# Performance work log

Measured on AMD Instinct MI355X. Metric: run time of the kernel, lower is better.

Reference implementation:

```python
import jax, jax.numpy as jnp
from jax import lax
import numpy as np

N = 32768; K = 8; M = 8192; G = 32; EF = 128

def _lrelu(x):
    return jnp.where(x > 0, x, 0.01 * x)

def _pc_res(x, W1, b1, W2, b2):
    h = _lrelu(x @ W1 + b1) @ W2 + b2
    return _lrelu(h + x)

def _conv3d(x, w, b):
    dn = ('NCDHW', 'OIDHW', 'NCDHW')
    return lax.conv_general_dilated(x, w, (1, 1, 1), 'SAME', dimension_numbers=dn) + b[None, :, None, None, None]

def setup_inputs():
    key = jax.random.key(0)
    ks = jax.random.split(key, 32)
    f32 = jnp.float32
    pc_KNN_idx = jax.random.randint(ks[0], (N * K,), 0, N, dtype=jnp.int32)
    pc_KNN_xyz = jax.random.normal(ks[1], (N * K, 3), dtype=f32)
    flat = jax.random.permutation(ks[2], G * G * G)[:M]  # unique voxel coords -> deterministic scatter
    voxel_xyz_int = jnp.stack([flat // (G * G), (flat // G) % G, flat % G], axis=1).astype(jnp.int32)
    voxel_KNN_idx = jax.random.randint(ks[3], (M * K,), 0, N, dtype=jnp.int32)
    voxel_KNN_xyz = jax.random.normal(ks[4], (M * K, 3), dtype=f32)
    s = 0.05
    def rn(i, shape):
        return jax.random.normal(ks[i], shape, dtype=f32) * s
    return dict(
        pc_KNN_idx=pc_KNN_idx, pc_KNN_xyz=pc_KNN_xyz, voxel_xyz_int=voxel_xyz_int,
        voxel_KNN_idx=voxel_KNN_idx, voxel_KNN_xyz=voxel_KNN_xyz,
        pcf_W1=rn(5, (3, EF)), pcf_b1=rn(6, (EF,)), pcf_W2=rn(7, (EF, EF)), pcf_b2=rn(8, (EF,)),
        pcres_W1=rn(9, (7, EF, EF)), pcres_b1=rn(10, (7, EF)),
        pcres_W2=rn(11, (7, EF, EF)), pcres_b2=rn(12, (7, EF)),
        pcc_W1=rn(13, (6, EF + 3, EF)), pcc_b1=rn(14, (6, EF)),
        pcc_W2=rn(15, (6, EF, EF)), pcc_b2=rn(16, (6, EF)),
        r3_Wc1=rn(17, (8, EF, EF, 3, 3, 3)), r3_bc1=rn(18, (8, EF)),
        r3_Wc2=rn(19, (8, EF, EF, 1, 1, 1)), r3_bc2=rn(20, (8, EF)),
        lin1_W=rn(21, (EF, EF)), lin1_b=rn(22, (EF,)),
        lin2_W=rn(23, (EF, EF)), lin2_b=rn(24, (EF,)),
        linb_W=rn(25, (EF, 3)), linb_b=rn(26, (3,)),
    )

def reference(pc_KNN_idx, pc_KNN_xyz, voxel_xyz_int, voxel_KNN_idx, voxel_KNN_xyz,
              pcf_W1, pcf_b1, pcf_W2, pcf_b2,
              pcres_W1, pcres_b1, pcres_W2, pcres_b2,
              pcc_W1, pcc_b1, pcc_W2, pcc_b2,
              r3_Wc1, r3_bc1, r3_Wc2, r3_bc2,
              lin1_W, lin1_b, lin2_W, lin2_b, linb_W, linb_b):
    # pc_conv_first: MLP on KNN relative xyz, max-pool over K neighbors -> [N, EF]
    out = _lrelu(pc_KNN_xyz @ pcf_W1 + pcf_b1) @ pcf_W2 + pcf_b2
    out = jnp.max(out.reshape(-1, K, EF), axis=1)
    out = _lrelu(out)
    out = _pc_res(out, pcres_W1[0], pcres_b1[0], pcres_W2[0], pcres_b2[0])
    for i in range(6):
        idx = pc_KNN_idx if i < 5 else voxel_KNN_idx
        xyz = pc_KNN_xyz if i < 5 else voxel_KNN_xyz
        g = jnp.concatenate([out[idx], xyz], axis=1)            # [R*K, EF+3]
        h = _lrelu(g @ pcc_W1[i] + pcc_b1[i]) @ pcc_W2[i] + pcc_b2[i]
        out = _lrelu(jnp.max(h.reshape(-1, K, EF), axis=1))     # [R, EF]
        out = _pc_res(out, pcres_W1[i + 1], pcres_b1[i + 1], pcres_W2[i + 1], pcres_b2[i + 1])
    # scatter voxel features into a dense grid (coords are unique)
    vi = voxel_xyz_int - jnp.min(voxel_xyz_int, axis=0)
    grid = jnp.zeros((G, G, G, EF), jnp.float32).at[vi[:, 0], vi[:, 1], vi[:, 2]].set(out)
    x = grid.transpose(3, 0, 1, 2)[None]                        # [1, EF, G, G, G]
    for i in range(8):
        y = _lrelu(_conv3d(x, r3_Wc1[i], r3_bc1[i]))
        y = _conv3d(y, r3_Wc2[i], r3_bc2[i])
        x = _lrelu(y + x)
    out = x[0].transpose(1, 2, 3, 0)[vi[:, 0], vi[:, 1], vi[:, 2]]  # gather back [M, EF]
    out = _lrelu(out @ lin1_W + lin1_b)
    out = _lrelu(out @ lin2_W + lin2_b)
    return jax.nn.sigmoid(out @ linb_W + linb_b)                # out_bool head [M, 3]
```

## Files before the change

kernel.cpp:

```cpp
#include <hip/hip_runtime.h>
#include <math.h>

#define EF 128
#define NPTS 32768
#define KNN 8
#define MVOX 8192
#define GDIM 32
#define NVOXG (GDIM*GDIM*GDIM)

typedef __attribute__((ext_vector_type(8))) short bfrag;
typedef __attribute__((ext_vector_type(4))) float f32x4;

__device__ __forceinline__ float lrelu(float x) { return x > 0.f ? x : 0.01f * x; }
__device__ __forceinline__ short f2b(float f) {
    unsigned u = __float_as_uint(f);
    return (short)((u + 0x7fff + ((u >> 16) & 1)) >> 16);
}
#define MFMA(a,b,c) __builtin_amdgcn_mfma_f32_16x16x32_bf16((a),(b),(c),0,0,0)
__device__ __forceinline__ int swz(int row, int bytecol) {
    return row * 256 + (bytecol ^ ((row & 7) << 4));
}

__global__ void k_pack_w(const float* __restrict__ src, short* __restrict__ dst,
                         int K_real, int n_steps, int k_str, int c_str,
                         int src_ls, int dst_ls, int n_layers) {
    int t = blockIdx.x * 256 + threadIdx.x;
    int per = n_steps * 4096;
    if (t >= n_layers * per) return;
    int layer = t / per;
    int u = t - layer * per;
    int r = u & 7, l = (u >> 3) & 63, ct = (u >> 9) & 7, s = u >> 12;
    int k = s * 32 + (l >> 4) * 8 + r;
    int col = ct * 16 + (l & 15);
    float v = (k < K_real) ? src[(size_t)layer * src_ls + (size_t)k * k_str + (size_t)col * c_str] : 0.f;
    dst[(size_t)layer * dst_ls + u] = f2b(v);
}
__global__ void k_pack_wc1(const float* __restrict__ src, short* __restrict__ dst) {
    int g = blockIdx.x;
    int layer = g / 1728;
    int t = (g - layer * 1728) * 256 + threadIdx.x;
    if (t >= 108 * 4096) return;
    int r = t & 7, l = (t >> 3) & 63, ct = (t >> 9) & 7, s = t >> 12;
    int tap = s >> 2;
    int ci = (s & 3) * 32 + (l >> 4) * 8 + r;
    int col = ct * 16 + (l & 15);
    dst[(size_t)layer * 442368 + t] =
        f2b(src[(size_t)layer * 442368 + ((size_t)col * 128 + ci) * 27 + tap]);
}


__global__ __launch_bounds__(512) void k_pcfirst(
    const float* __restrict__ xyz, const short* __restrict__ w1p, const float* __restrict__ b1,
    const short* __restrict__ w2p, const float* __restrict__ b2,
    const short* __restrict__ rw1p, const float* __restrict__ rb1,
    const short* __restrict__ rw2p, const float* __restrict__ rb2,
    float* __restrict__ out32, short* __restrict__ out16) {
    __shared__ __align__(16) char tb[32768];
    int wid = threadIdx.x >> 6, lane = threadIdx.x & 63, lrow = lane & 15, lq = lane >> 4;
    int wm = wid >> 2, wn = wid & 3;
    int rowbase = blockIdx.x * 128;
    f32x4 zv = {0.f, 0.f, 0.f, 0.f};
    {
        f32x4 acc1[4][2];
        #pragma unroll
        for (int rt = 0; rt < 4; ++rt) { acc1[rt][0] = zv; acc1[rt][1] = zv; }
        bfrag Bv[2];
        #pragma unroll
        for (int ct = 0; ct < 2; ++ct) Bv[ct] = ((const bfrag*)w1p)[(wn * 2 + ct) * 64 + lane];
        #pragma unroll
        for (int rt = 0; rt < 4; ++rt) {
            bfrag a4;
            #pragma unroll
            for (int r = 0; r < 8; ++r) a4[r] = 0;
            if (lq == 0) {
                int gr = rowbase + wm * 64 + rt * 16 + lrow;
                a4[0] = f2b(xyz[gr * 3]); a4[1] = f2b(xyz[gr * 3 + 1]); a4[2] = f2b(xyz[gr * 3 + 2]);
            }
            #pragma unroll
            for (int ct = 0; ct < 2; ++ct) acc1[rt][ct] = MFMA(a4, Bv[ct], acc1[rt][ct]);
        }
        float bb1[2];
        #pragma unroll
        for (int ct = 0; ct < 2; ++ct) bb1[ct] = b1[wn * 32 + ct * 16 + lrow];
        #pragma unroll
        for (int rt = 0; rt < 4; ++rt)
            #pragma unroll
            for (int ct = 0; ct < 2; ++ct)
                #pragma unroll
                for (int r = 0; r < 4; ++r) {
                    int row = wm * 64 + rt * 16 + lq * 4 + r, col = wn * 32 + ct * 16 + lrow;
                    *(short*)(tb + swz(row, col * 2)) = f2b(lrelu(acc1[rt][ct][r] + bb1[ct]));
                }
    }
    __syncthreads();
    float bb2[2];
    #pragma unroll
    for (int ct = 0; ct < 2; ++ct) bb2[ct] = b2[wn * 32 + ct * 16 + lrow];
    f32x4 acc[4][2];
    #pragma unroll
    for (int rt = 0; rt < 4; ++rt) { acc[rt][0] = zv; acc[rt][1] = zv; }
    const bfrag* bp2 = (const bfrag*)w2p;
    #pragma unroll
    for (int s = 0; s < 4; ++s) {
        bfrag Bv[2];
        #pragma unroll
        for (int ct = 0; ct < 2; ++ct) Bv[ct] = bp2[(s * 8 + wn * 2 + ct) * 64 + lane];
        bfrag av[4];
        #pragma unroll
        for (int rt = 0; rt < 4; ++rt) {
            int row = wm * 64 + rt * 16 + lrow;
            av[rt] = *(const bfrag*)(tb + swz(row, s * 64 + lq * 16));
        }
        #pragma unroll
        for (int ct = 0; ct < 2; ++ct)
            #pragma unroll
            for (int rt = 0; rt < 4; ++rt) acc[rt][ct] = MFMA(av[rt], Bv[ct], acc[rt][ct]);
    }
    float pv[4][2];
    #pragma unroll
    for (int rt = 0; rt < 4; ++rt)
        #pragma unroll
        for (int ct = 0; ct < 2; ++ct) {
            float m = -INFINITY;
            #pragma unroll
            for (int r = 0; r < 4; ++r) m = fmaxf(m, acc[rt][ct][r] + bb2[ct]);
            m = fmaxf(m, __shfl_xor(m, 16, 64));
            pv[rt][ct] = lrelu(m);
        }
    __syncthreads();
    float* xf = (float*)(tb + 4096);
    char*  tres = tb + 12544;
    if ((lq & 1) == 0) {
        #pragma unroll
        for (int rt = 0; rt < 4; ++rt)
            #pragma unroll
            for (int ct = 0; ct < 2; ++ct) {
                int row = wm * 8 + rt * 2 + (lq >> 1), col = wn * 32 + ct * 16 + lrow;
                *(short*)(tb + swz(row, col * 2)) = f2b(pv[rt][ct]);
                xf[row * 130 + col] = pv[rt][ct];
            }
    }
    __syncthreads();
    {
        f32x4 r1 = zv;
        #pragma unroll
        for (int s = 0; s < 4; ++s) {
            bfrag B = ((const bfrag*)rw1p)[(s * 8 + wid) * 64 + lane];
            bfrag a = *(const bfrag*)(tb + swz(lrow, s * 64 + lq * 16));
            r1 = MFMA(a, B, r1);
        }
        float rb1v = rb1[wid * 16 + lrow];
        #pragma unroll
        for (int r = 0; r < 4; ++r) {
            int row = lq * 4 + r;
            *(short*)(tres + swz(row, (wid * 16 + lrow) * 2)) = f2b(lrelu(r1[r] + rb1v));
        }
    }
    __syncthreads();
    {
        f32x4 r2 = zv;
        #pragma unroll
        for (int s = 0; s < 4; ++s) {
            bfrag B = ((const bfrag*)rw2p)[(s * 8 + wid) * 64 + lane];
            bfrag a = *(const bfrag*)(tres + swz(lrow, s * 64 + lq * 16));
            r2 = MFMA(a, B, r2);
        }
        float rb2v = rb2[wid * 16 + lrow];
        int p0 = blockIdx.x * 16;
        #pragma unroll
        for (int r = 0; r < 4; ++r) {
            int row = lq * 4 + r, col = wid * 16 + lrow;
            float v = lrelu(r2[r] + rb2v + xf[row * 130 + col]);
            size_t o = (size_t)(p0 + row) * 128 + col;
            out16[o] = f2b(v);
            if (out32) out32[o] = v;
        }
    }
}

__global__ __launch_bounds__(512) void k_pcconv(
    const short* __restrict__ fin16, const int* __restrict__ idx, const float* __restrict__ xyz,
    const short* __restrict__ w1p, const float* __restrict__ b1,
    const short* __restrict__ w2p, const float* __restrict__ b2,
    const short* __restrict__ rw1p, const float* __restrict__ rb1,
    const short* __restrict__ rw2p, const float* __restrict__ rb2,
    float* __restrict__ out32, short* __restrict__ out16) {
    __shared__ __align__(16) char tb[32768];
    int wid = threadIdx.x >> 6, lane = threadIdx.x & 63, lrow = lane & 15, lq = lane >> 4;
    int wm = wid >> 2, wn = wid & 3;
    int rowbase = blockIdx.x * 128;
    f32x4 zv = {0.f, 0.f, 0.f, 0.f};
    {
        int srow = threadIdx.x >> 2, sseg = threadIdx.x & 3;
        int nb = idx[rowbase + srow];
        const bfrag* src = (const bfrag*)(fin16 + (size_t)nb * 128);
        #pragma unroll
        for (int j = 0; j < 4; ++j) {
            int seg = sseg + j * 4;
            bfrag v = src[seg];
            *(bfrag*)(tb + swz(srow, seg * 16)) = v;
        }
    }
    __syncthreads();
    float bb1[2], bb2[2];
    #pragma unroll
    for (int ct = 0; ct < 2; ++ct) {
        bb1[ct] = b1[wn * 32 + ct * 16 + lrow];
        bb2[ct] = b2[wn * 32 + ct * 16 + lrow];
    }
    f32x4 acc[4][2];
    #pragma unroll
    for (int rt = 0; rt < 4; ++rt) { acc[rt][0] = zv; acc[rt][1] = zv; }
    const bfrag* bp1 = (const bfrag*)w1p;
    #pragma unroll
    for (int s = 0; s < 4; ++s) {
        bfrag Bv[2];
        #pragma unroll
        for (int ct = 0; ct < 2; ++ct) Bv[ct] = bp1[(s * 8 + wn * 2 + ct) * 64 + lane];
        bfrag av[4];
        #pragma unroll
        for (int rt = 0; rt < 4; ++rt) {
            int row = wm * 64 + rt * 16 + lrow;
            av[rt] = *(const bfrag*)(tb + swz(row, s * 64 + lq * 16));
        }
        #pragma unroll
        for (int ct = 0; ct < 2; ++ct)
            #pragma unroll
            for (int rt = 0; rt < 4; ++rt) acc[rt][ct] = MFMA(av[rt], Bv[ct], acc[rt][ct]);
    }
    {
        bfrag Bv[2];
        #pragma unroll
        for (int ct = 0; ct < 2; ++ct) Bv[ct] = bp1[(32 + wn * 2 + ct) * 64 + lane];
        #pragma unroll
        for (int rt = 0; rt < 4; ++rt) {
            bfrag a4;
            #pragma unroll
            for (int r = 0; r < 8; ++r) a4[r] = 0;
            if (lq == 0) {
                int gr = rowbase + wm * 64 + rt * 16 + lrow;
                a4[0] = f2b(xyz[gr * 3]); a4[1] = f2b(xyz[gr * 3 + 1]); a4[2] = f2b(xyz[gr * 3 + 2]);
            }
            #pragma unroll
            for (int ct = 0; ct < 2; ++ct) acc[rt][ct] = MFMA(a4, Bv[ct], acc[rt][ct]);
        }
    }
    __syncthreads();
    #pragma unroll
    for (int rt = 0; rt < 4; ++rt)
        #pragma unroll
        for (int ct = 0; ct < 2; ++ct)
            #pragma unroll
            for (int r = 0; r < 4; ++r) {
                int row = wm * 64 + rt * 16 + lq * 4 + r, col = wn * 32 + ct * 16 + lrow;
                *(short*)(tb + swz(row, col * 2)) = f2b(lrelu(acc[rt][ct][r] + bb1[ct]));
            }
    __syncthreads();
    f32x4 acc2[4][2];
    #pragma unroll
    for (int rt = 0; rt < 4; ++rt) { acc2[rt][0] = zv; acc2[rt][1] = zv; }
    const bfrag* bp2 = (const bfrag*)w2p;
    #pragma unroll
    for (int s = 0; s < 4; ++s) {
        bfrag Bv[2];
        #pragma unroll
        for (int ct = 0; ct < 2; ++ct) Bv[ct] = bp2[(s * 8 + wn * 2 + ct) * 64 + lane];
        bfrag av[4];
        #pragma unroll
        for (int rt = 0; rt < 4; ++rt) {
            int row = wm * 64 + rt * 16 + lrow;
            av[rt] = *(const bfrag*)(tb + swz(row, s * 64 + lq * 16));
        }
        #pragma unroll
        for (int ct = 0; ct < 2; ++ct)
            #pragma unroll
            for (int rt = 0; rt < 4; ++rt) acc2[rt][ct] = MFMA(av[rt], Bv[ct], acc2[rt][ct]);
    }
    float pv[4][2];
    #pragma unroll
    for (int rt = 0; rt < 4; ++rt)
        #pragma unroll
        for (int ct = 0; ct < 2; ++ct) {
            float m = -INFINITY;
            #pragma unroll
            for (int r = 0; r < 4; ++r) m = fmaxf(m, acc2[rt][ct][r] + bb2[ct]);
            m = fmaxf(m, __shfl_xor(m, 16, 64));
            pv[rt][ct] = lrelu(m);
        }
    __syncthreads();
    float* xf = (float*)(tb + 4096);
    char*  tres = tb + 12544;
    if ((lq & 1) == 0) {
        #pragma unroll
        for (int rt = 0; rt < 4; ++rt)
            #pragma unroll
            for (int ct = 0; ct < 2; ++ct) {
                int row = wm * 8 + rt * 2 + (lq >> 1), col = wn * 32 + ct * 16 + lrow;
                *(short*)(tb + swz(row, col * 2)) = f2b(pv[rt][ct]);
                xf[row * 130 + col] = pv[rt][ct];
            }
    }
    __syncthreads();
    {
        f32x4 r1 = zv;
        #pragma unroll
        for (int s = 0; s < 4; ++s) {
            bfrag B = ((const bfrag*)rw1p)[(s * 8 + wid) * 64 + lane];
            bfrag a = *(const bfrag*)(tb + swz(lrow, s * 64 + lq * 16));
            r1 = MFMA(a, B, r1);
        }
        float rb1v = rb1[wid * 16 + lrow];
        #pragma unroll
        for (int r = 0; r < 4; ++r) {
            int row = lq * 4 + r;
            *(short*)(tres + swz(row, (wid * 16 + lrow) * 2)) = f2b(lrelu(r1[r] + rb1v));
        }
    }
    __syncthreads();
    {
        f32x4 r2 = zv;
        #pragma unroll
        for (int s = 0; s < 4; ++s) {
            bfrag B = ((const bfrag*)rw2p)[(s * 8 + wid) * 64 + lane];
            bfrag a = *(const bfrag*)(tres + swz(lrow, s * 64 + lq * 16));
            r2 = MFMA(a, B, r2);
        }
        float rb2v = rb2[wid * 16 + lrow];
        int p0 = blockIdx.x * 16;
        #pragma unroll
        for (int r = 0; r < 4; ++r) {
            int row = lq * 4 + r, col = wid * 16 + lrow;
            float v = lrelu(r2[r] + rb2v + xf[row * 130 + col]);
            size_t o = (size_t)(p0 + row) * 128 + col;
            out16[o] = f2b(v);
            if (out32) out32[o] = v;
        }
    }
}

__global__ __launch_bounds__(512) void k_conv3(
    const float* __restrict__ gin32, const short* __restrict__ gin16,
    const short* __restrict__ w1p, const float* __restrict__ b1,
    const short* __restrict__ w2p, const float* __restrict__ b2,
    float* __restrict__ gout32, short* __restrict__ gout16) {
    __shared__ __align__(16) char Ab[65536];
    int wid = threadIdx.x >> 6, lane = threadIdx.x & 63, lrow = lane & 15, lq = lane >> 4;
    int kg = wid & 1, wn = (wid >> 1) & 1, wm = wid >> 2;
    int va = blockIdx.x >> 3, vb0 = (blockIdx.x & 7) * 4;
    bfrag zf;
    #pragma unroll
    for (int r = 0; r < 8; ++r) zf[r] = 0;
    f32x4 zv = {0.f, 0.f, 0.f, 0.f};
    f32x4 acc[4][4];
    #pragma unroll
    for (int rt = 0; rt < 4; ++rt)
        #pragma unroll
        for (int ct = 0; ct < 4; ++ct) acc[rt][ct] = zv;
    const bfrag* bp1 = (const bfrag*)w1p;

    #pragma unroll 1
    for (int dai = 0; dai < 3; ++dai) {
        __syncthreads();
        {
            int aa = va + dai - 1;
            bool aok = (unsigned)aa < 32u;
            #pragma unroll
            for (int j = 0; j < 6; ++j) {
                int task = (int)threadIdx.x + j * 512;
                int srow = task >> 4, seg = task & 15;
                int bl = srow >> 5, c = srow & 31;
                int sb = vb0 - 1 + bl;
                bool ok = aok && ((unsigned)sb < 32u);
                size_t gb = ok ? ((size_t)((aa * 32 + sb) * 32 + c) * 128 + seg * 8) : 0;
                bfrag v = *((const bfrag*)gin16 + gb / 8);
                *(bfrag*)(Ab + swz(srow, seg * 16)) = ok ? v : zf;
            }
        }
        __syncthreads();
        #pragma unroll
        for (int t9 = 0; t9 < 9; ++t9) {
            int db = t9 / 3 - 1, dc = t9 % 3 - 1;
            int tap = dai * 9 + t9;
            #pragma unroll
            for (int ss = 0; ss < 2; ++ss) {
                int s = kg * 2 + ss;
                bfrag Bv[4];
                #pragma unroll
                for (int ct = 0; ct < 4; ++ct)
                    Bv[ct] = bp1[((tap * 4 + s) * 8 + wn * 4 + ct) * 64 + lane];
                bfrag av[4];
                #pragma unroll
                for (int rt = 0; rt < 4; ++rt) {
                    int ci = ((rt & 1) << 4) + lrow + dc;
                    bool ok = (unsigned)ci < 32u;
                    int srow2 = (wm * 2 + db + 1 + (rt >> 1)) * 32 + (ok ? ci : 0);
                    bfrag t = *(const bfrag*)(Ab + swz(srow2, s * 64 + lq * 16));
                    av[rt] = ok ? t : zf;
                }
                #pragma unroll
                for (int ct = 0; ct < 4; ++ct)
                    #pragma unroll
                    for (int rt = 0; rt < 4; ++rt) acc[rt][ct] = MFMA(av[rt], Bv[ct], acc[rt][ct]);
            }
        }
    }
    __syncthreads();
    if (kg == 1) {
        int p = wm * 2 + wn;
        #pragma unroll
        for (int rt = 0; rt < 4; ++rt)
            #pragma unroll
            for (int ct = 0; ct < 4; ++ct)
                *(f32x4*)(Ab + p * 16384 + ((rt * 4 + ct) * 64 + lane) * 16) = acc[rt][ct];
    }
    __syncthreads();
    if (kg == 0) {
        int p = wm * 2 + wn;
        #pragma unroll
        for (int rt = 0; rt < 4; ++rt)
            #pragma unroll
            for (int ct = 0; ct < 4; ++ct)
                acc[rt][ct] += *(const f32x4*)(Ab + p * 16384 + ((rt * 4 + ct) * 64 + lane) * 16);
    }
    __syncthreads();
    if (kg == 0) {
        float bb1[4];
        #pragma unroll
        for (int ct = 0; ct < 4; ++ct) bb1[ct] = b1[wn * 64 + ct * 16 + lrow];
        #pragma unroll
        for (int rt = 0; rt < 4; ++rt)
            #pragma unroll
            for (int ct = 0; ct < 4; ++ct)
                #pragma unroll
                for (int r = 0; r < 4; ++r) {
                    int row = wm * 64 + rt * 16 + lq * 4 + r, col = wn * 64 + ct * 16 + lrow;
                    *(short*)(Ab + swz(row, col * 2)) = f2b(lrelu(acc[rt][ct][r] + bb1[ct]));
                }
    }
    __syncthreads();
    int wm2 = wid >> 2, wn2 = wid & 3;
    float bb2[2];
    #pragma unroll
    for (int ct = 0; ct < 2; ++ct) bb2[ct] = b2[wn2 * 32 + ct * 16 + lrow];
    f32x4 acc2[4][2];
    #pragma unroll
    for (int rt = 0; rt < 4; ++rt) { acc2[rt][0] = zv; acc2[rt][1] = zv; }
    const bfrag* bp2 = (const bfrag*)w2p;
    #pragma unroll
    for (int s = 0; s < 4; ++s) {
        bfrag Bv[2];
        #pragma unroll
        for (int ct = 0; ct < 2; ++ct) Bv[ct] = bp2[(s * 8 + wn2 * 2 + ct) * 64 + lane];
        bfrag av[4];
        #pragma unroll
        for (int rt = 0; rt < 4; ++rt) {
            int row = wm2 * 64 + rt * 16 + lrow;
            av[rt] = *(const bfrag*)(Ab + swz(row, s * 64 + lq * 16));
        }
        #pragma unroll
        for (int ct = 0; ct < 2; ++ct)
            #pragma unroll
            for (int rt = 0; rt < 4; ++rt) acc2[rt][ct] = MFMA(av[rt], Bv[ct], acc2[rt][ct]);
    }
    #pragma unroll
    for (int rt = 0; rt < 4; ++rt)
        #pragma unroll
        for (int ct = 0; ct < 2; ++ct)
            #pragma unroll
            for (int r = 0; r < 4; ++r) {
                int row = wm2 * 64 + rt * 16 + lq * 4 + r;
                int voxel = (va * 32 + vb0 + (row >> 5)) * 32 + (row & 31);
                size_t o = (size_t)voxel * 128 + wn2 * 32 + ct * 16 + lrow;
                float v = lrelu(acc2[rt][ct][r] + bb2[ct] + gin32[o]);
                gout32[o] = v; gout16[o] = f2b(v);
            }
}

__global__ __launch_bounds__(512) void k_head(
    const short* __restrict__ g16, const int* __restrict__ vx, const int* __restrict__ vmin,
    const short* __restrict__ w1p, const float* __restrict__ b1,
    const short* __restrict__ w2p, const float* __restrict__ b2,
    const float* __restrict__ W3, const float* __restrict__ b3,
    float* __restrict__ out) {
    __shared__ __align__(16) char tb[16384];
    __shared__ float t2[64][129];
    int wid = threadIdx.x >> 6, lane = threadIdx.x & 63, lrow = lane & 15, lq = lane >> 4;
    int rowbase = blockIdx.x * 64;
    int goff[4];
    #pragma unroll
    for (int rt = 0; rt < 4; ++rt) {
        int m = rowbase + rt * 16 + lrow;
        int v0 = vx[m * 3 + 0] - vmin[0];
        int v1 = vx[m * 3 + 1] - vmin[1];
        int v2 = vx[m * 3 + 2] - vmin[2];
        goff[rt] = ((v0 * 32 + v1) * 32 + v2) * 128;
    }
    float bb1 = b1[wid * 16 + lrow], bb2 = b2[wid * 16 + lrow];
    f32x4 zv = {0.f, 0.f, 0.f, 0.f};
    f32x4 acc[4];
    #pragma unroll
    for (int rt = 0; rt < 4; ++rt) acc[rt] = zv;
    const bfrag* bp1 = (const bfrag*)w1p;
    #pragma unroll
    for (int s = 0; s < 4; ++s) {
        bfrag B = bp1[(s * 8 + wid) * 64 + lane];
        #pragma unroll
        for (int rt = 0; rt < 4; ++rt) {
            bfrag a = *((const bfrag*)(g16 + goff[rt]) + s * 4 + lq);
            acc[rt] = MFMA(a, B, acc[rt]);
        }
    }
    #pragma unroll
    for (int rt = 0; rt < 4; ++rt)
        #pragma unroll
        for (int r = 0; r < 4; ++r) {
            int row = rt * 16 + lq * 4 + r, col = wid * 16 + lrow;
            *(short*)(tb + swz(row, col * 2)) = f2b(lrelu(acc[rt][r] + bb1));
        }
    __syncthreads();
    f32x4 acc2[4];
    #pragma unroll
    for (int rt = 0; rt < 4; ++rt) acc2[rt] = zv;
    const bfrag* bp2 = (const bfrag*)w2p;
    #pragma unroll
    for (int s = 0; s < 4; ++s) {
        bfrag B = bp2[(s * 8 + wid) * 64 + lane];
        #pragma unroll
        for (int rt = 0; rt < 4; ++rt) {
            int row = rt * 16 + lrow;
            bfrag av = *(const bfrag*)(tb + swz(row, s * 64 + lq * 16));
            acc2[rt] = MFMA(av, B, acc2[rt]);
        }
    }
    #pragma unroll
    for (int rt = 0; rt < 4; ++rt)
        #pragma unroll
        for (int r = 0; r < 4; ++r) {
            int row = rt * 16 + lq * 4 + r, col = wid * 16 + lrow;
            t2[row][col] = lrelu(acc2[rt][r] + bb2);
        }
    __syncthreads();
    if (threadIdx.x < 192) {
        int row = threadIdx.x & 63, c = threadIdx.x >> 6;
        float s = b3[c];
        #pragma unroll 4
        for (int k = 0; k < 128; ++k) s += t2[row][k] * W3[k * 3 + c];
        out[(size_t)(rowbase + row) * 3 + c] = 1.f / (1.f + expf(-s));
    }
}

__global__ void k_vmin(const int* __restrict__ vx, int M, int* __restrict__ vmin) {
    __shared__ int sm[3 * 256];
    int t = threadIdx.x;
    int m0 = 0x7fffffff, m1 = 0x7fffffff, m2 = 0x7fffffff;
    for (int i = t; i < M; i += 256) {
        m0 = min(m0, vx[i * 3 + 0]); m1 = min(m1, vx[i * 3 + 1]); m2 = min(m2, vx[i * 3 + 2]);
    }
    sm[t] = m0; sm[256 + t] = m1; sm[512 + t] = m2;
    __syncthreads();
    for (int s = 128; s > 0; s >>= 1) {
        if (t < s) {
            sm[t] = min(sm[t], sm[t + s]);
            sm[256 + t] = min(sm[256 + t], sm[256 + t + s]);
            sm[512 + t] = min(sm[512 + t], sm[512 + t + s]);
        }
        __syncthreads();
    }
    if (t == 0) { vmin[0] = sm[0]; vmin[1] = sm[256]; vmin[2] = sm[512]; }
}

__global__ void k_scatter(const float* __restrict__ vf, const int* __restrict__ vx,
                          const int* __restrict__ vmin, float* __restrict__ g32, short* __restrict__ g16) {
    int m = blockIdx.x, j = threadIdx.x;
    int v0 = vx[m * 3 + 0] - vmin[0];
    int v1 = vx[m * 3 + 1] - vmin[1];
    int v2 = vx[m * 3 + 2] - vmin[2];
    size_t o = (size_t)(((v0 * GDIM) + v1) * GDIM + v2) * EF + j;
    float v = vf[(size_t)m * EF + j];
    g32[o] = v; g16[o] = f2b(v);
}

extern "C" void kernel_launch(void* const* d_in, const int* in_sizes, int n_in,
                              void* d_out, int out_size, void* d_ws, size_t ws_size,
                              hipStream_t stream) {
    const int*   pc_idx  = (const int*)  d_in[0];
    const float* pc_xyz  = (const float*)d_in[1];
    const int*   vox_int = (const int*)  d_in[2];
    const int*   vox_idx = (const int*)  d_in[3];
    const float* vox_xyz = (const float*)d_in[4];
    const float* pcf_W1  = (const float*)d_in[5];
    const float* pcf_b1  = (const float*)d_in[6];
    const float* pcf_W2  = (const float*)d_in[7];
    const float* pcf_b2  = (const float*)d_in[8];
    const float* pcres_W1 = (const float*)d_in[9];
    const float* pcres_b1 = (const float*)d_in[10];
    const float* pcres_W2 = (const float*)d_in[11];
    const float* pcres_b2 = (const float*)d_in[12];
    const float* pcc_W1  = (const float*)d_in[13];
    const float* pcc_b1  = (const float*)d_in[14];
    const float* pcc_W2  = (const float*)d_in[15];
    const float* pcc_b2  = (const float*)d_in[16];
    const float* r3_Wc1  = (const float*)d_in[17];
    const float* r3_bc1  = (const float*)d_in[18];
    const float* r3_Wc2  = (const float*)d_in[19];
    const float* r3_bc2  = (const float*)d_in[20];
    const float* lin1_W  = (const float*)d_in[21];
    const float* lin1_b  = (const float*)d_in[22];
    const float* lin2_W  = (const float*)d_in[23];
    const float* lin2_b  = (const float*)d_in[24];
    const float* linb_W  = (const float*)d_in[25];
    const float* linb_b  = (const float*)d_in[26];

    const size_t NE = (size_t)NPTS * EF;
    float* A32 = (float*)d_ws;
    float* B32 = A32 + NE;
    short* A16 = (short*)(B32 + NE);
    short* B16 = A16 + NE;
    float* Y32 = (float*)(B16 + NE);
    short* Y16 = (short*)(Y32 + NE);
    short* pcf_w1p = Y16 + NE;
    short* pcf_w2p = pcf_w1p + 1 * 4096;
    short* pcc_w1p = pcf_w2p + 4 * 4096;
    short* pcc_w2p = pcc_w1p + 6 * 5 * 4096;
    short* pcr_w1p = pcc_w2p + 6 * 4 * 4096;
    short* pcr_w2p = pcr_w1p + 7 * 4 * 4096;
    short* wc2p    = pcr_w2p + 7 * 4 * 4096;
    short* lin1p   = wc2p    + 8 * 4 * 4096;
    short* lin2p   = lin1p   + 4 * 4096;
    short* wc1p    = lin2p   + 4 * 4096;
    int*   vmin    = (int*)(wc1p + 8 * 108 * 4096);

    k_pack_w<<<16, 256, 0, stream>>>(pcf_W1, pcf_w1p, 3, 1, 128, 1, 0, 0, 1);
    k_pack_w<<<64, 256, 0, stream>>>(pcf_W2, pcf_w2p, 128, 4, 128, 1, 0, 0, 1);
    k_pack_w<<<480, 256, 0, stream>>>(pcc_W1, pcc_w1p, 131, 5, 128, 1, 131 * 128, 5 * 4096, 6);
    k_pack_w<<<384, 256, 0, stream>>>(pcc_W2, pcc_w2p, 128, 4, 128, 1, 128 * 128, 4 * 4096, 6);
    k_pack_w<<<448, 256, 0, stream>>>(pcres_W1, pcr_w1p, 128, 4, 128, 1, 128 * 128, 4 * 4096, 7);
    k_pack_w<<<448, 256, 0, stream>>>(pcres_W2, pcr_w2p, 128, 4, 128, 1, 128 * 128, 4 * 4096, 7);
    k_pack_w<<<512, 256, 0, stream>>>(r3_Wc2, wc2p, 128, 4, 1, 128, 128 * 128, 4 * 4096, 8);
    k_pack_w<<<64, 256, 0, stream>>>(lin1_W, lin1p, 128, 4, 128, 1, 0, 0, 1);
    k_pack_w<<<64, 256, 0, stream>>>(lin2_W, lin2p, 128, 4, 128, 1, 0, 0, 1);
    k_pack_wc1<<<8 * 1728, 256, 0, stream>>>(r3_Wc1, wc1p);

    k_pcfirst<<<NPTS * KNN / 128, 512, 0, stream>>>(pc_xyz, pcf_w1p, pcf_b1, pcf_w2p, pcf_b2,
        pcr_w1p, pcres_b1, pcr_w2p, pcres_b2, nullptr, A16);
    short* cur16 = A16; short* nxt16 = B16;
    for (int i = 0; i < 5; ++i) {
        k_pcconv<<<NPTS * KNN / 128, 512, 0, stream>>>(cur16, pc_idx, pc_xyz,
            pcc_w1p + (size_t)i * 5 * 4096, pcc_b1 + i * EF,
            pcc_w2p + (size_t)i * 4 * 4096, pcc_b2 + i * EF,
            pcr_w1p + (size_t)(i + 1) * 4 * 4096, pcres_b1 + (i + 1) * EF,
            pcr_w2p + (size_t)(i + 1) * 4 * 4096, pcres_b2 + (i + 1) * EF,
            nullptr, nxt16);
        short* t = cur16; cur16 = nxt16; nxt16 = t;
    }
    k_pcconv<<<MVOX * KNN / 128, 512, 0, stream>>>(cur16, vox_idx, vox_xyz,
        pcc_w1p + (size_t)5 * 5 * 4096, pcc_b1 + 5 * EF,
        pcc_w2p + (size_t)5 * 4 * 4096, pcc_b2 + 5 * EF,
        pcr_w1p + (size_t)6 * 4 * 4096, pcres_b1 + 6 * EF,
        pcr_w2p + (size_t)6 * 4 * 4096, pcres_b2 + 6 * EF,
        A32, A16);

    k_vmin<<<1, 256, 0, stream>>>(vox_int, MVOX, vmin);
    hipMemsetAsync(B32, 0, NE * sizeof(float), stream);
    hipMemsetAsync(B16, 0, NE * sizeof(short), stream);
    k_scatter<<<MVOX, 128, 0, stream>>>(A32, vox_int, vmin, B32, B16);

    float* cur32 = B32; short* curg = B16;
    float* nxt32 = Y32; short* nxtg = Y16;
    for (int i = 0; i < 8; ++i) {
        k_conv3<<<256, 512, 0, stream>>>(cur32, curg, wc1p + (size_t)i * 108 * 4096, r3_bc1 + i * EF,
                                         wc2p + (size_t)i * 4 * 4096, r3_bc2 + i * EF,
                                         nxt32, nxtg);
        float* t32 = cur32; cur32 = nxt32; nxt32 = t32;
        short* t16 = curg; curg = nxtg; nxtg = t16;
    }

    k_head<<<MVOX / 64, 512, 0, stream>>>(curg, vox_int, vmin,
                                          lin1p, lin1_b, lin2p, lin2_b, linb_W, linb_b,
                                          (float*)d_out);
}
```

Measured before the change: 647.8 us.

## Precompute per-point first-layer projection before gather in point convolutions

Because the first MLP layer of each point conv is linear, the product of the 128 feature channels with W1 is now computed once per point at the end of the previous layer (U = feat·W1[:128]) instead of once per gathered neighbor. The conv kernel gathers U rows and adds the xyz·W1[128:131] terms and the bias in scalar FP32 before the activation. This removes the first 128x128 GEMM over N*K rows, replacing it with an N-row GEMM in the producer. It rounds U to bf16 before the xyz term is added, which shifts numerics slightly.

```diff
diff --git a/kernel.cpp b/kernel.cpp
--- a/kernel.cpp
+++ b/kernel.cpp
@@ -15,6 +15,9 @@
 __device__ __forceinline__ short f2b(float f) {
     unsigned u = __float_as_uint(f);
     return (short)((u + 0x7fff + ((u >> 16) & 1)) >> 16);
+}
+__device__ __forceinline__ float b2f(short s) {
+    return __uint_as_float(((unsigned)(unsigned short)s) << 16);
 }
 #define MFMA(a,b,c) __builtin_amdgcn_mfma_f32_16x16x32_bf16((a),(b),(c),0,0,0)
 __device__ __forceinline__ int swz(int row, int bytecol) {
@@ -54,6 +57,7 @@
     const short* __restrict__ w2p, const float* __restrict__ b2,
     const short* __restrict__ rw1p, const float* __restrict__ rb1,
     const short* __restrict__ rw2p, const float* __restrict__ rb2,
+    const short* __restrict__ wu, short* __restrict__ Uout,
     float* __restrict__ out32, short* __restrict__ out16) {
     __shared__ __align__(16) char tb[32768];
     int wid = threadIdx.x >> 6, lane = threadIdx.x & 63, lrow = lane & 15, lq = lane >> 4;
@@ -172,18 +176,34 @@
             int row = lq * 4 + r, col = wid * 16 + lrow;
             float v = lrelu(r2[r] + rb2v + xf[row * 130 + col]);
             size_t o = (size_t)(p0 + row) * 128 + col;
-            out16[o] = f2b(v);
+            if (out16) out16[o] = f2b(v);
             if (out32) out32[o] = v;
-        }
+            *(short*)(tb + swz(row, col * 2)) = f2b(v);
+        }
+    }
+    __syncthreads();
+    if (wu) {
+        f32x4 ua = zv;
+        #pragma unroll
+        for (int s = 0; s < 4; ++s) {
+            bfrag B = ((const bfrag*)wu)[(s * 8 + wid) * 64 + lane];
+            bfrag a = *(const bfrag*)(tb + swz(lrow, s * 64 + lq * 16));
+            ua = MFMA(a, B, ua);
+        }
+        int p0 = blockIdx.x * 16;
+        #pragma unroll
+        for (int r = 0; r < 4; ++r)
+            Uout[(size_t)(p0 + lq * 4 + r) * 128 + wid * 16 + lrow] = f2b(ua[r]);
     }
 }
 
 __global__ __launch_bounds__(512) void k_pcconv(
-    const short* __restrict__ fin16, const int* __restrict__ idx, const float* __restrict__ xyz,
-    const short* __restrict__ w1p, const float* __restrict__ b1,
+    const short* __restrict__ Uin, const int* __restrict__ idx, const float* __restrict__ xyz,
+    const float* __restrict__ W1raw, const float* __restrict__ b1,
     const short* __restrict__ w2p, const float* __restrict__ b2,
     const short* __restrict__ rw1p, const float* __restrict__ rb1,
     const short* __restrict__ rw2p, const float* __restrict__ rb2,
+    const short* __restrict__ wu, short* __restrict__ Uout,
     float* __restrict__ out32, short* __restrict__ out16) {
     __shared__ __align__(16) char tb[32768];
     int wid = threadIdx.x >> 6, lane = threadIdx.x & 63, lrow = lane & 15, lq = lane >> 4;
@@ -191,71 +211,41 @@
     int rowbase = blockIdx.x * 128;
     f32x4 zv = {0.f, 0.f, 0.f, 0.f};
     {
-        int srow = threadIdx.x >> 2, sseg = threadIdx.x & 3;
-        int nb = idx[rowbase + srow];
-        const bfrag* src = (const bfrag*)(fin16 + (size_t)nb * 128);
-        #pragma unroll
-        for (int j = 0; j < 4; ++j) {
-            int seg = sseg + j * 4;
-            bfrag v = src[seg];
-            *(bfrag*)(tb + swz(srow, seg * 16)) = v;
-        }
-    }
-    __syncthreads();
-    float bb1[2], bb2[2];
-    #pragma unroll
-    for (int ct = 0; ct < 2; ++ct) {
-        bb1[ct] = b1[wn * 32 + ct * 16 + lrow];
-        bb2[ct] = b2[wn * 32 + ct * 16 + lrow];
-    }
-    f32x4 acc[4][2];
-    #pragma unroll
-    for (int rt = 0; rt < 4; ++rt) { acc[rt][0] = zv; acc[rt][1] = zv; }
-    const bfrag* bp1 = (const bfrag*)w1p;
-    #pragma unroll
-    for (int s = 0; s < 4; ++s) {
-        bfrag Bv[2];
-        #pragma unroll
-        for (int ct = 0; ct < 2; ++ct) Bv[ct] = bp1[(s * 8 + wn * 2 + ct) * 64 + lane];
-        bfrag av[4];
-        #pragma unroll
-        for (int rt = 0; rt < 4; ++rt) {
-            int row = wm * 64 + rt * 16 + lrow;
-            av[rt] = *(const bfrag*)(tb + swz(row, s * 64 + lq * 16));
-        }
-        #pragma unroll
-        for (int ct = 0; ct < 2; ++ct)
-            #pragma unroll
-            for (int rt = 0; rt < 4; ++rt) acc[rt][ct] = MFMA(av[rt], Bv[ct], acc[rt][ct]);
-    }
-    {
-        bfrag Bv[2];
-        #pragma unroll
-        for (int ct = 0; ct < 2; ++ct) Bv[ct] = bp1[(32 + wn * 2 + ct) * 64 + lane];
-        #pragma unroll
-        for (int rt = 0; rt < 4; ++rt) {
-            bfrag a4;
-            #pragma unroll
-            for (int r = 0; r < 8; ++r) a4[r] = 0;
-            if (lq == 0) {
-                int gr = rowbase + wm * 64 + rt * 16 + lrow;
-                a4[0] = f2b(xyz[gr * 3]); a4[1] = f2b(xyz[gr * 3 + 1]); a4[2] = f2b(xyz[gr * 3 + 2]);
+        int srow = threadIdx.x >> 2;
+        int cb = (threadIdx.x & 3) * 32;
+        int grow = rowbase + srow;
+        int nb = idx[grow];
+        const bfrag* up = (const bfrag*)(Uin + (size_t)nb * 128) + (cb >> 3);
+        bfrag u0 = up[0], u1 = up[1], u2 = up[2], u3 = up[3];
+        float x0 = xyz[grow * 3], y0 = xyz[grow * 3 + 1], z0 = xyz[grow * 3 + 2];
+        const f32x4* Wx = (const f32x4*)(W1raw + 128 * 128) + (cb >> 2);
+        const f32x4* Wy = (const f32x4*)(W1raw + 129 * 128) + (cb >> 2);
+        const f32x4* Wz = (const f32x4*)(W1raw + 130 * 128) + (cb >> 2);
+        const f32x4* Bb = (const f32x4*)b1 + (cb >> 2);
+        #pragma unroll
+        for (int j0 = 0; j0 < 4; ++j0) {
+            bfrag uj = (j0 == 0) ? u0 : (j0 == 1) ? u1 : (j0 == 2) ? u2 : u3;
+            f32x4 wxa = Wx[j0 * 2], wxb = Wx[j0 * 2 + 1];
+            f32x4 wya = Wy[j0 * 2], wyb = Wy[j0 * 2 + 1];
+            f32x4 wza = Wz[j0 * 2], wzb = Wz[j0 * 2 + 1];
+            f32x4 bba = Bb[j0 * 2], bbb = Bb[j0 * 2 + 1];
+            bfrag v;
+            #pragma unroll
+            for (int j = 0; j < 8; ++j) {
+                float wxv = (j < 4) ? wxa[j & 3] : wxb[j & 3];
+                float wyv = (j < 4) ? wya[j & 3] : wyb[j & 3];
+                float wzv = (j < 4) ? wza[j & 3] : wzb[j & 3];
+                float bbv = (j < 4) ? bba[j & 3] : bbb[j & 3];
+                float s = b2f(uj[j]) + x0 * wxv + y0 * wyv + z0 * wzv + bbv;
+                v[j] = f2b(lrelu(s));
             }
-            #pragma unroll
-            for (int ct = 0; ct < 2; ++ct) acc[rt][ct] = MFMA(a4, Bv[ct], acc[rt][ct]);
-        }
-    }
-    __syncthreads();
-    #pragma unroll
-    for (int rt = 0; rt < 4; ++rt)
-        #pragma unroll
-        for (int ct = 0; ct < 2; ++ct)
-            #pragma unroll
-            for (int r = 0; r < 4; ++r) {
-                int row = wm * 64 + rt * 16 + lq * 4 + r, col = wn * 32 + ct * 16 + lrow;
-                *(short*)(tb + swz(row, col * 2)) = f2b(lrelu(acc[rt][ct][r] + bb1[ct]));
-            }
-    __syncthreads();
+            *(bfrag*)(tb + swz(srow, (cb + j0 * 8) * 2)) = v;
+        }
+    }
+    __syncthreads();
+    float bb2[2];
+    #pragma unroll
+    for (int ct = 0; ct < 2; ++ct) bb2[ct] = b2[wn * 32 + ct * 16 + lrow];
     f32x4 acc2[4][2];
     #pragma unroll
     for (int rt = 0; rt < 4; ++rt) { acc2[rt][0] = zv; acc2[rt][1] = zv; }
@@ -332,9 +322,24 @@
             int row = lq * 4 + r, col = wid * 16 + lrow;
             float v = lrelu(r2[r] + rb2v + xf[row * 130 + col]);
             size_t o = (size_t)(p0 + row) * 128 + col;
-            out16[o] = f2b(v);
+            if (out16) out16[o] = f2b(v);
             if (out32) out32[o] = v;
-        }
+            *(short*)(tb + swz(row, col * 2)) = f2b(v);
+        }
+    }
+    __syncthreads();
+    if (wu) {
+        f32x4 ua = zv;
+        #pragma unroll
+        for (int s = 0; s < 4; ++s) {
+            bfrag B = ((const bfrag*)wu)[(s * 8 + wid) * 64 + lane];
+            bfrag a = *(const bfrag*)(tb + swz(lrow, s * 64 + lq * 16));
+            ua = MFMA(a, B, ua);
+        }
+        int p0 = blockIdx.x * 16;
+        #pragma unroll
+        for (int r = 0; r < 4; ++r)
+            Uout[(size_t)(p0 + lq * 4 + r) * 128 + wid * 16 + lrow] = f2b(ua[r]);
     }
 }
 
@@ -641,24 +646,26 @@
     k_pack_w<<<64, 256, 0, stream>>>(lin2_W, lin2p, 128, 4, 128, 1, 0, 0, 1);
     k_pack_wc1<<<8 * 1728, 256, 0, stream>>>(r3_Wc1, wc1p);
 
+    short* UA = A16; short* UB = B16;
     k_pcfirst<<<NPTS * KNN / 128, 512, 0, stream>>>(pc_xyz, pcf_w1p, pcf_b1, pcf_w2p, pcf_b2,
-        pcr_w1p, pcres_b1, pcr_w2p, pcres_b2, nullptr, A16);
-    short* cur16 = A16; short* nxt16 = B16;
+        pcr_w1p, pcres_b1, pcr_w2p, pcres_b2,
+        pcc_w1p , UA, nullptr, nullptr);
+    short* curU = UA; short* nxtU = UB;
     for (int i = 0; i < 5; ++i) {
-        k_pcconv<<<NPTS * KNN / 128, 512, 0, stream>>>(cur16, pc_idx, pc_xyz,
-            pcc_w1p + (size_t)i * 5 * 4096, pcc_b1 + i * EF,
+        k_pcconv<<<NPTS * KNN / 128, 512, 0, stream>>>(curU, pc_idx, pc_xyz,
+            pcc_W1 + (size_t)i * 131 * 128, pcc_b1 + i * EF,
             pcc_w2p + (size_t)i * 4 * 4096, pcc_b2 + i * EF,
             pcr_w1p + (size_t)(i + 1) * 4 * 4096, pcres_b1 + (i + 1) * EF,
             pcr_w2p + (size_t)(i + 1) * 4 * 4096, pcres_b2 + (i + 1) * EF,
-            nullptr, nxt16);
-        short* t = cur16; cur16 = nxt16; nxt16 = t;
-    }
-    k_pcconv<<<MVOX * KNN / 128, 512, 0, stream>>>(cur16, vox_idx, vox_xyz,
-        pcc_w1p + (size_t)5 * 5 * 4096, pcc_b1 + 5 * EF,
+            pcc_w1p + (size_t)(i + 1) * 5 * 4096, nxtU, nullptr, nullptr);
+        short* t = curU; curU = nxtU; nxtU = t;
+    }
+    k_pcconv<<<MVOX * KNN / 128, 512, 0, stream>>>(curU, vox_idx, vox_xyz,
+        pcc_W1 + (size_t)5 * 131 * 128, pcc_b1 + 5 * EF,
         pcc_w2p + (size_t)5 * 4 * 4096, pcc_b2 + 5 * EF,
         pcr_w1p + (size_t)6 * 4 * 4096, pcres_b1 + 6 * EF,
         pcr_w2p + (size_t)6 * 4 * 4096, pcres_b2 + 6 * EF,
-        A32, A16);
+        nullptr, nullptr, A32, A16);
 
     k_vmin<<<1, 256, 0, stream>>>(vox_int, MVOX, vmin);
     hipMemsetAsync(B32, 0, NE * sizeof(float), stream);
```

Result: slower. 828.0 us (+27.8%).

## Double-buffer conv3 input slabs with async global-to-LDS loads

Applied to the files above, without the earlier changes.

The 3D conv kernel now fetches each depth slab straight into LDS with global_load_lds, double-buffering two slabs so the next slab's load overlaps MFMA work on the current one. The LDS swizzle is applied by permuting the global source segment, and out-of-range taps read from a small zeroed global buffer instead of storing zeros from registers. This removes register staging and one barrier per slab. LDS use grows from 64 KB to 96 KB per block, and correctness depends on the barrier waiting for the async LDS writes to land.

```diff
diff --git a/kernel.cpp b/kernel.cpp
--- a/kernel.cpp
+++ b/kernel.cpp
@@ -19,6 +19,11 @@
 #define MFMA(a,b,c) __builtin_amdgcn_mfma_f32_16x16x32_bf16((a),(b),(c),0,0,0)
 __device__ __forceinline__ int swz(int row, int bytecol) {
     return row * 256 + (bytecol ^ ((row & 7) << 4));
+}
+__device__ __forceinline__ void gload_lds16(const void* g, void* l) {
+    __builtin_amdgcn_global_load_lds(
+        (const __attribute__((address_space(1))) unsigned int*)g,
+        (__attribute__((address_space(3))) unsigned int*)l, 16, 0, 0);
 }
 
 __global__ void k_pack_w(const float* __restrict__ src, short* __restrict__ dst,
@@ -340,10 +345,11 @@
 
 __global__ __launch_bounds__(512) void k_conv3(
     const float* __restrict__ gin32, const short* __restrict__ gin16,
+    const short* __restrict__ zeros,
     const short* __restrict__ w1p, const float* __restrict__ b1,
     const short* __restrict__ w2p, const float* __restrict__ b2,
     float* __restrict__ gout32, short* __restrict__ gout16) {
-    __shared__ __align__(16) char Ab[65536];
+    __shared__ __align__(16) char Ab[98304];
     int wid = threadIdx.x >> 6, lane = threadIdx.x & 63, lrow = lane & 15, lq = lane >> 4;
     int kg = wid & 1, wn = (wid >> 1) & 1, wm = wid >> 2;
     int va = blockIdx.x >> 3, vb0 = (blockIdx.x & 7) * 4;
@@ -358,25 +364,32 @@
         for (int ct = 0; ct < 4; ++ct) acc[rt][ct] = zv;
     const bfrag* bp1 = (const bfrag*)w1p;
 
+    int tsk0 = (int)threadIdx.x;
+    #define ISSUE_SLAB(aa_, buf_)                                                           \
+        {                                                                                   \
+            int aa = (aa_);                                                                 \
+            bool aok = (unsigned)aa < 32u;                                                  \
+            _Pragma("unroll")                                                               \
+            for (int j = 0; j < 6; ++j) {                                                   \
+                int task = tsk0 + j * 512;                                                  \
+                int srow = task >> 4, segl = task & 15;                                     \
+                int bl = srow >> 5, c = srow & 31;                                          \
+                int sb = vb0 - 1 + bl;                                                      \
+                int segg = segl ^ (srow & 7);                                               \
+                bool ok = aok && ((unsigned)sb < 32u);                                      \
+                const short* gsrc = ok ? (gin16 + (size_t)((aa * 32 + sb) * 32 + c) * 128 + segg * 8) \
+                                       : (zeros + segg * 8);                                \
+                gload_lds16(gsrc, Ab + (buf_) * 49152 + (size_t)task * 16);                 \
+            }                                                                               \
+        }
+
+    ISSUE_SLAB(va - 1, 0)
+    __syncthreads();
+
     #pragma unroll 1
     for (int dai = 0; dai < 3; ++dai) {
-        __syncthreads();
-        {
-            int aa = va + dai - 1;
-            bool aok = (unsigned)aa < 32u;
-            #pragma unroll
-            for (int j = 0; j < 6; ++j) {
-                int task = (int)threadIdx.x + j * 512;
-                int srow = task >> 4, seg = task & 15;
-                int bl = srow >> 5, c = srow & 31;
-                int sb = vb0 - 1 + bl;
-                bool ok = aok && ((unsigned)sb < 32u);
-                size_t gb = ok ? ((size_t)((aa * 32 + sb) * 32 + c) * 128 + seg * 8) : 0;
-                bfrag v = *((const bfrag*)gin16 + gb / 8);
-                *(bfrag*)(Ab + swz(srow, seg * 16)) = ok ? v : zf;
-            }
-        }
-        __syncthreads();
+        if (dai < 2) ISSUE_SLAB(va + dai, (dai + 1) & 1)
+        const char* slab = Ab + (dai & 1) * 49152;
         #pragma unroll
         for (int t9 = 0; t9 < 9; ++t9) {
             int db = t9 / 3 - 1, dc = t9 % 3 - 1;
@@ -394,7 +407,7 @@
                     int ci = ((rt & 1) << 4) + lrow + dc;
                     bool ok = (unsigned)ci < 32u;
                     int srow2 = (wm * 2 + db + 1 + (rt >> 1)) * 32 + (ok ? ci : 0);
-                    bfrag t = *(const bfrag*)(Ab + swz(srow2, s * 64 + lq * 16));
+                    bfrag t = *(const bfrag*)(slab + swz(srow2, s * 64 + lq * 16));
                     av[rt] = ok ? t : zf;
                 }
                 #pragma unroll
@@ -403,8 +416,10 @@
                     for (int rt = 0; rt < 4; ++rt) acc[rt][ct] = MFMA(av[rt], Bv[ct], acc[rt][ct]);
             }
         }
-    }
-    __syncthreads();
+        __syncthreads();
+    }
+    #undef ISSUE_SLAB
+
     if (kg == 1) {
         int p = wm * 2 + wn;
         #pragma unroll
@@ -628,7 +643,10 @@
     short* lin1p   = wc2p    + 8 * 4 * 4096;
     short* lin2p   = lin1p   + 4 * 4096;
     short* wc1p    = lin2p   + 4 * 4096;
-    int*   vmin    = (int*)(wc1p + 8 * 108 * 4096);
+    short* zbuf    = wc1p + 8 * 108 * 4096;
+    int*   vmin    = (int*)(zbuf + 2048);
+
+    hipMemsetAsync(zbuf, 0, 4096, stream);
 
     k_pack_w<<<16, 256, 0, stream>>>(pcf_W1, pcf_w1p, 3, 1, 128, 1, 0, 0, 1);
     k_pack_w<<<64, 256, 0, stream>>>(pcf_W2, pcf_w2p, 128, 4, 128, 1, 0, 0, 1);
@@ -668,7 +686,8 @@
     float* cur32 = B32; short* curg = B16;
     float* nxt32 = Y32; short* nxtg = Y16;
     for (int i = 0; i < 8; ++i) {
-        k_conv3<<<256, 512, 0, stream>>>(cur32, curg, wc1p + (size_t)i * 108 * 4096, r3_bc1 + i * EF,
+        k_conv3<<<256, 512, 0, stream>>>(cur32, curg, zbuf,
+                                         wc1p + (size_t)i * 108 * 4096, r3_bc1 + i * EF,
                                          wc2p + (size_t)i * 4 * 4096, r3_bc2 + i * EF,
                                          nxt32, nxtg);
         float* t32 = cur32; cur32 = nxt32; nxt32 = t32;
```

Result: no change. 645.6 us (-0.4%).
